# Kernel tuning notes

Measured on AMD Instinct MI355X. Metric: run time of the kernel, lower is better.

The kernel has to match this reference:

```python
import jax, jax.numpy as jnp
import numpy as np

BN_EPS = 1e-5
NEG_SLOPE = 0.2


def _bn(h, gamma, beta, axes):
    # training-mode batch norm over given axes; channels on last axis
    mu = jnp.mean(h, axis=axes, keepdims=True)
    var = jnp.var(h, axis=axes, keepdims=True)
    return (h - mu) * jax.lax.rsqrt(var + BN_EPS) * gamma + beta


def _leaky(h):
    return jnp.where(h >= 0, h, NEG_SLOPE * h)


def setup_inputs() -> dict:
    key = jax.random.key(0)
    k0, k1, k2, k3 = jax.random.split(key, 4)
    B, N, C, K, M = 8, 1024, 512, 20, 64  # M = dim // downrate
    x = jax.random.normal(k0, (B, N, C), dtype=jnp.float32)
    idx = jax.random.randint(k1, (B, N, K), 0, N, dtype=jnp.int32)
    W1 = jax.random.normal(k2, (M, 2 * C), dtype=jnp.float32) * (1.0 / np.sqrt(2 * C))
    gamma1 = jnp.ones((M,), jnp.float32)
    beta1 = jnp.zeros((M,), jnp.float32)
    W2 = jax.random.normal(k3, (C, M), dtype=jnp.float32) * (1.0 / np.sqrt(M))
    gamma2 = jnp.ones((C,), jnp.float32)
    beta2 = jnp.zeros((C,), jnp.float32)
    return dict(x=x, idx=idx, W1=W1, gamma1=gamma1, beta1=beta1,
                W2=W2, gamma2=gamma2, beta2=beta2)


def reference(x, idx, W1, gamma1, beta1, W2, gamma2, beta2):
    # x: (B, N, C) point features; idx: (B, N, K) neighbor indices into N
    neigh = jax.vmap(lambda xb, ib: xb[ib])(x, idx)          # (B, N, K, C) gather
    center = x[:, :, None, :]                                 # (B, N, 1, C)
    # get_graph_feature: concat(feature - x, x) -> channels = 2C
    edge = jnp.concatenate(
        [neigh - center, jnp.broadcast_to(center, neigh.shape)], axis=-1)  # (B,N,K,2C)
    # conv1: 1x1 conv == per-edge linear, then BN2d (stats over B,N,K) + LeakyReLU
    h = jnp.einsum('bnkc,mc->bnkm', edge, W1)                 # (B, N, K, M)
    h = _leaky(_bn(h, gamma1, beta1, (0, 1, 2)))
    # max-aggregate over neighbors
    h = jnp.max(h, axis=2)                                    # (B, N, M)
    # conv2: 1x1 conv1d, BN1d (stats over B,N) + LeakyReLU
    h2 = jnp.einsum('bnm,dm->bnd', h, W2)                     # (B, N, C)
    h2 = _leaky(_bn(h2, gamma2, beta2, (0, 1)))
    return h2  # (B, N, dim), matches final permute(0, 2, 1)
```

## Files before the change

kernel.cpp:

```cpp
#include <hip/hip_runtime.h>
#include <math.h>

#define B_ 8
#define N_ 1024
#define C_ 512
#define K_ 20
#define M_ 64
#define R_ (B_*N_)

typedef short bf16x8 __attribute__((ext_vector_type(8)));
typedef float f32x4  __attribute__((ext_vector_type(4)));

#define WS_Y     0
#define WS_HMM   (WS_Y + R_*64)
#define WS_P1A   (WS_HMM + R_*64)
#define WS_P2A   (WS_P1A + 128)
#define WS_HB    (WS_P2A + 1024)

__device__ __forceinline__ uint f2b(float f) {
    union { float f; uint u; } v; v.f = f;
    return (v.u + 0x7fffu + ((v.u >> 16) & 1u)) >> 16;
}
__device__ __forceinline__ uint2 f4_to_b4(float4 v) {
    uint2 r;
    r.x = f2b(v.x) | (f2b(v.y) << 16);
    r.y = f2b(v.z) | (f2b(v.w) << 16);
    return r;
}
__device__ __forceinline__ float bits2f(uint u) {
    union { uint u; float f; } v; v.u = u; return v.f;
}
__device__ __forceinline__ float lrelu(float v) { return v >= 0.f ? v : 0.2f * v; }

__global__ __launch_bounds__(256) void k_yz(const float* __restrict__ x,
                                            const float* __restrict__ W1,
                                            ushort* __restrict__ Y,
                                            float* __restrict__ P1a,
                                            float* __restrict__ P2a) {
    __shared__ __align__(16) ushort sWb[65536];
    const int t = threadIdx.x, lane = t & 63, w = t >> 6;
    const int wr = w >> 1, wc = w & 1;
    const int r0 = blockIdx.x * 32;

#pragma unroll 8
    for (int i = 0; i < 32; ++i) {
        const int f = i * 256 + t;
        const int j = f >> 6, kq = f & 63;
        const float* src = (j < 64) ? &W1[(size_t)j * 1024 + kq * 8]
                                    : &W1[(size_t)(j - 64) * 1024 + 512 + kq * 8];
        const float4 a = *(const float4*)src;
        const float4 b = *(const float4*)(src + 4);
        const uint2 la = f4_to_b4(a), lb = f4_to_b4(b);
        uint4 v; v.x = la.x; v.y = la.y; v.z = lb.x; v.w = lb.y;
        const int off = j * 1024 + ((kq * 16) ^ ((j & 7) << 4));
        *(uint4*)((char*)sWb + off) = v;
    }
    if (blockIdx.x == 0 && t < 128) P1a[t] = 0.f;
    if (blockIdx.x >= 1 && blockIdx.x <= 4) P2a[(blockIdx.x - 1) * 256 + t] = 0.f;

    const int arow = r0 + wr * 16 + (lane & 15);
    const size_t xbase = (size_t)arow * 512 + ((lane >> 4) * 8);
    float4 xr[8][4];
#pragma unroll
    for (int ks = 0; ks < 8; ++ks) {
        const size_t b = xbase + ks * 64;
        xr[ks][0] = *(const float4*)&x[b];
        xr[ks][1] = *(const float4*)&x[b + 4];
        xr[ks][2] = *(const float4*)&x[b + 32];
        xr[ks][3] = *(const float4*)&x[b + 36];
    }

    f32x4 acc[4];
#pragma unroll
    for (int jj = 0; jj < 4; ++jj) acc[jj] = (f32x4){0.f, 0.f, 0.f, 0.f};

    __syncthreads();

    const int jbase = wc * 64 + (lane & 15);
    const int kb_base = (lane >> 4) * 16;

#pragma unroll
    for (int ks = 0; ks < 8; ++ks) {
        const uint2 c00 = f4_to_b4(xr[ks][0]), c01 = f4_to_b4(xr[ks][1]);
        const uint2 c10 = f4_to_b4(xr[ks][2]), c11 = f4_to_b4(xr[ks][3]);
        union { uint4 u; bf16x8 b; } A0, A1;
        A0.u.x = c00.x; A0.u.y = c00.y; A0.u.z = c01.x; A0.u.w = c01.y;
        A1.u.x = c10.x; A1.u.y = c10.y; A1.u.z = c11.x; A1.u.w = c11.y;
        const int k0 = ks * 128 + kb_base;
#pragma unroll
        for (int jj = 0; jj < 4; ++jj) {
            const int jrow = jbase + jj * 16;
            const int rowoff = jrow * 1024;
            const int sw = (jrow & 7) << 4;
            const bf16x8 B0 = *(const bf16x8*)((char*)sWb + rowoff + (k0 ^ sw));
            const bf16x8 B1 = *(const bf16x8*)((char*)sWb + rowoff + ((k0 + 64) ^ sw));
            acc[jj] = __builtin_amdgcn_mfma_f32_16x16x32_bf16(A0.b, B0, acc[jj], 0, 0, 0);
            acc[jj] = __builtin_amdgcn_mfma_f32_16x16x32_bf16(A1.b, B1, acc[jj], 0, 0, 0);
        }
    }

    const int crow = r0 + wr * 16 + (lane >> 4) * 4;
    const int ccol = wc * 64 + (lane & 15);
#pragma unroll
    for (int jj = 0; jj < 4; ++jj)
#pragma unroll
        for (int i = 0; i < 4; ++i)
            Y[(size_t)(crow + i) * 128 + ccol + jj * 16] = (ushort)f2b(acc[jj][i]);
}

__global__ __launch_bounds__(256) void k_gather(const ushort* __restrict__ Y,
                                                const int* __restrict__ idx,
                                                uint* __restrict__ HMM,
                                                float* __restrict__ P1a) {
    __shared__ float sSum[8][64];
    __shared__ float sQ[8][64];
    const int t = threadIdx.x, lane = t & 63, w = t >> 6;
    const int sub = lane >> 5, c = lane & 31;
    const int grp = w * 2 + sub;
    const uint* Yu = (const uint*)Y;
    float sum0 = 0.f, sum1 = 0.f, sq0 = 0.f, sq1 = 0.f;

#pragma unroll
    for (int pi = 0; pi < 4; ++pi) {
        const int p = blockIdx.x * 32 + w * 8 + pi * 2 + sub;
        const int bb = p >> 10;
        const uint ysu = Yu[(size_t)p * 64 + c];
        const uint zsu = Yu[(size_t)p * 64 + 32 + c];
        const float base0 = bits2f(zsu << 16) - bits2f(ysu << 16);
        const float base1 = bits2f(zsu & 0xffff0000u) - bits2f(ysu & 0xffff0000u);
        float mx0 = -INFINITY, mx1 = -INFINITY, mn0 = INFINITY, mn1 = INFINITY;
        int4 j4[5];
#pragma unroll
        for (int q = 0; q < 5; ++q) j4[q] = *(const int4*)&idx[p * 20 + q * 4];
#pragma unroll
        for (int k = 0; k < 20; ++k) {
            const int j = ((const int*)j4)[k];
            const uint yg = Yu[(size_t)(bb * 1024 + j) * 64 + c];
            const float h0 = bits2f(yg << 16) + base0;
            const float h1 = bits2f(yg & 0xffff0000u) + base1;
            sum0 += h0; sum1 += h1;
            sq0 += h0 * h0; sq1 += h1 * h1;
            mx0 = fmaxf(mx0, h0); mx1 = fmaxf(mx1, h1);
            mn0 = fminf(mn0, h0); mn1 = fminf(mn1, h1);
        }
        uint2 st;
        st.x = f2b(mx0) | (f2b(mn0) << 16);
        st.y = f2b(mx1) | (f2b(mn1) << 16);
        *(uint2*)&HMM[(size_t)p * 64 + 2 * c] = st;
    }

    *(float2*)&sSum[grp][2 * c] = make_float2(sum0, sum1);
    *(float2*)&sQ[grp][2 * c]   = make_float2(sq0, sq1);
    __syncthreads();
    if (t < 64) {
        float s = 0.f, q = 0.f;
#pragma unroll
        for (int g = 0; g < 8; ++g) { s += sSum[g][t]; q += sQ[g][t]; }
        atomicAdd(&P1a[t], s);
        atomicAdd(&P1a[64 + t], q);
    }
}

__global__ __launch_bounds__(256) void k_qsum(const uint* __restrict__ HMM,
                                              const float* __restrict__ P1a,
                                              const float* __restrict__ g1,
                                              const float* __restrict__ b1,
                                              const float* __restrict__ W2,
                                              ushort* __restrict__ Hb,
                                              float* __restrict__ P2a) {
    __shared__ float sSc1[64], sSh1[64];
    const int t = threadIdx.x, lane = t & 63, w = t >> 6;
    if (t < 64) {
        const float inv = 1.f / (float)(R_ * K_);
        const float mu  = P1a[t] * inv;
        const float var = P1a[64 + t] * inv - mu * mu;
        const float rs  = rsqrtf(var + 1e-5f);
        const float sc  = g1[t] * rs;
        sSc1[t] = sc;
        sSh1[t] = b1[t] - mu * sc;
    }
    __syncthreads();

    const int rtile = blockIdx.x, half = blockIdx.y;
    const int r0 = rtile * 64;
    const int dsub = half * 256 + w * 64;
    const int qd = lane >> 4, s = lane & 15;
    const int mc0 = qd * 8;

    bf16x8 bfr[4][2];
#pragma unroll
    for (int f = 0; f < 4; ++f) {
        const int d = dsub + f * 16 + s;
#pragma unroll
        for (int g = 0; g < 2; ++g) {
            const float4 wa = *(const float4*)&W2[(size_t)d * 64 + mc0 + g * 32];
            const float4 wb = *(const float4*)&W2[(size_t)d * 64 + mc0 + g * 32 + 4];
            const uint2 lo = f4_to_b4(wa), hi = f4_to_b4(wb);
            union { uint4 u; bf16x8 b; } cv;
            cv.u.x = lo.x; cv.u.y = lo.y; cv.u.z = hi.x; cv.u.w = hi.y;
            bfr[f][g] = cv.b;
        }
    }

    f32x4 acc[4][4];
#pragma unroll
    for (int rt = 0; rt < 4; ++rt)
#pragma unroll
        for (int f = 0; f < 4; ++f) acc[rt][f] = (f32x4){0.f,0.f,0.f,0.f};

#pragma unroll
    for (int rt = 0; rt < 4; ++rt) {
        const int row = r0 + rt * 16 + s;
#pragma unroll
        for (int g = 0; g < 2; ++g) {
            const int mc = mc0 + g * 32;
            const uint4 u0 = *(const uint4*)&HMM[(size_t)row * 64 + mc];
            const uint4 u1 = *(const uint4*)&HMM[(size_t)row * 64 + mc + 4];
            float v[8];
#pragma unroll
            for (int i = 0; i < 4; ++i) {
                const uint ua = ((const uint*)&u0)[i];
                const uint ub = ((const uint*)&u1)[i];
                const float c0 = sSc1[mc + i],     h0 = sSh1[mc + i];
                const float c4 = sSc1[mc + 4 + i], h4 = sSh1[mc + 4 + i];
                const float a0 = c0 >= 0.f ? bits2f(ua << 16) : bits2f(ua & 0xffff0000u);
                const float a4 = c4 >= 0.f ? bits2f(ub << 16) : bits2f(ub & 0xffff0000u);
                v[i]     = lrelu(a0 * c0 + h0);
                v[i + 4] = lrelu(a4 * c4 + h4);
            }
            uint4 pk;
            pk.x = f2b(v[0]) | (f2b(v[1]) << 16);
            pk.y = f2b(v[2]) | (f2b(v[3]) << 16);
            pk.z = f2b(v[4]) | (f2b(v[5]) << 16);
            pk.w = f2b(v[6]) | (f2b(v[7]) << 16);
            if (half == 0) *(uint4*)&Hb[(size_t)row * 64 + mc] = pk;
            union { uint4 u; bf16x8 b; } cv; cv.u = pk;
#pragma unroll
            for (int f = 0; f < 4; ++f)
                acc[rt][f] = __builtin_amdgcn_mfma_f32_16x16x32_bf16(cv.b, bfr[f][g], acc[rt][f], 0, 0, 0);
        }
    }

#pragma unroll
    for (int f = 0; f < 4; ++f) {
        float ss = 0.f, qq = 0.f;
#pragma unroll
        for (int rt = 0; rt < 4; ++rt)
#pragma unroll
            for (int i = 0; i < 4; ++i) {
                const float vv = acc[rt][f][i];
                ss += vv; qq += vv * vv;
            }
        ss += __shfl_xor(ss, 16); ss += __shfl_xor(ss, 32);
        qq += __shfl_xor(qq, 16); qq += __shfl_xor(qq, 32);
        if (lane < 16) {
            const int d = dsub + f * 16 + s;
            atomicAdd(&P2a[d], ss);
            atomicAdd(&P2a[512 + d], qq);
        }
    }
}

__global__ __launch_bounds__(256) void k_out(const ushort* __restrict__ Hb,
                                             const float* __restrict__ W2,
                                             const float* __restrict__ P2a,
                                             const float* __restrict__ g2,
                                             const float* __restrict__ b2,
                                             float* __restrict__ out) {
    __shared__ float sSc2[256], sSh2[256];
    const int t = threadIdx.x, lane = t & 63, w = t >> 6;
    const int rtile = blockIdx.x, half = blockIdx.y;
    {
        const int d = half * 256 + t;
        const float inv = 1.f / (float)R_;
        const float mu  = P2a[d] * inv;
        const float var = P2a[512 + d] * inv - mu * mu;
        const float rs  = rsqrtf(var + 1e-5f);
        const float sc  = g2[d] * rs;
        sSc2[t] = sc;
        sSh2[t] = b2[d] - mu * sc;
    }
    __syncthreads();

    const int r0 = rtile * 64;
    const int dsub = half * 256 + w * 64;
    const int qd = lane >> 4, s = lane & 15;
    const int mc0 = qd * 8;

    bf16x8 bfr[4][2];
#pragma unroll
    for (int f = 0; f < 4; ++f) {
        const int d = dsub + f * 16 + s;
#pragma unroll
        for (int g = 0; g < 2; ++g) {
            const float4 wa = *(const float4*)&W2[(size_t)d * 64 + mc0 + g * 32];
            const float4 wb = *(const float4*)&W2[(size_t)d * 64 + mc0 + g * 32 + 4];
            const uint2 lo = f4_to_b4(wa), hi = f4_to_b4(wb);
            union { uint4 u; bf16x8 b; } cv;
            cv.u.x = lo.x; cv.u.y = lo.y; cv.u.z = hi.x; cv.u.w = hi.y;
            bfr[f][g] = cv.b;
        }
    }

    f32x4 acc[4][4];
#pragma unroll
    for (int rt = 0; rt < 4; ++rt)
#pragma unroll
        for (int f = 0; f < 4; ++f) acc[rt][f] = (f32x4){0.f,0.f,0.f,0.f};

#pragma unroll
    for (int rt = 0; rt < 4; ++rt) {
        const int row = r0 + rt * 16 + s;
#pragma unroll
        for (int g = 0; g < 2; ++g) {
            const bf16x8 af = *(const bf16x8*)&Hb[(size_t)row * 64 + mc0 + g * 32];
#pragma unroll
            for (int f = 0; f < 4; ++f)
                acc[rt][f] = __builtin_amdgcn_mfma_f32_16x16x32_bf16(af, bfr[f][g], acc[rt][f], 0, 0, 0);
        }
    }

#pragma unroll
    for (int rt = 0; rt < 4; ++rt)
#pragma unroll
        for (int f = 0; f < 4; ++f) {
            const int dl = w * 64 + f * 16 + s;
            const float c2 = sSc2[dl], h2 = sSh2[dl];
            const int d = dsub + f * 16 + s;
#pragma unroll
            for (int i = 0; i < 4; ++i) {
                const float vv = lrelu(acc[rt][f][i] * c2 + h2);
                out[(size_t)(r0 + rt * 16 + qd * 4 + i) * 512 + d] = vv;
            }
        }
}

extern "C" void kernel_launch(void* const* d_in, const int* in_sizes, int n_in,
                              void* d_out, int out_size, void* d_ws, size_t ws_size,
                              hipStream_t stream) {
    const float* x   = (const float*)d_in[0];
    const int*   idx = (const int*)d_in[1];
    const float* W1  = (const float*)d_in[2];
    const float* g1  = (const float*)d_in[3];
    const float* b1  = (const float*)d_in[4];
    const float* W2  = (const float*)d_in[5];
    const float* g2  = (const float*)d_in[6];
    const float* b2  = (const float*)d_in[7];
    float* out = (float*)d_out;
    float* ws  = (float*)d_ws;

    ushort* Y    = (ushort*)(ws + WS_Y);
    uint*   HMM  = (uint*)(ws + WS_HMM);
    float*  P1a  = ws + WS_P1A;
    float*  P2a  = ws + WS_P2A;
    ushort* Hb   = (ushort*)(ws + WS_HB);

    k_yz    <<<dim3(R_ / 32), dim3(256), 0, stream>>>(x, W1, Y, P1a, P2a);
    k_gather<<<dim3(R_ / 32), dim3(256), 0, stream>>>(Y, idx, HMM, P1a);
    k_qsum  <<<dim3(128, 2),  dim3(256), 0, stream>>>(HMM, P1a, g1, b1, W2, Hb, P2a);
    k_out   <<<dim3(128, 2),  dim3(256), 0, stream>>>(Hb, W2, P2a, g2, b2, out);
}
```

Baseline: 52.32 us.

## Stream W1 in double-buffered K-chunks in k_yz with 512-thread blocks

The k_yz GEMM no longer stages the whole 128x512 bf16 W1 tile (128 KB LDS) up front. It now streams 64-wide K slices into a 32 KB double-buffered LDS ring, prefetching the next slice of W1 and x into registers while MFMAs run on the current one. Blocks grow to 512 threads (8 waves, each owning 32 output columns), which cuts LDS use and register pressure so more blocks can be resident. The cost is a __syncthreads per K step and fewer MFMAs per wave between barriers.

```diff
diff --git a/kernel.cpp b/kernel.cpp
--- a/kernel.cpp
+++ b/kernel.cpp
@@ -32,77 +32,116 @@
 }
 __device__ __forceinline__ float lrelu(float v) { return v >= 0.f ? v : 0.2f * v; }
 
-__global__ __launch_bounds__(256) void k_yz(const float* __restrict__ x,
+__global__ __launch_bounds__(512) void k_yz(const float* __restrict__ x,
                                             const float* __restrict__ W1,
                                             ushort* __restrict__ Y,
                                             float* __restrict__ P1a,
                                             float* __restrict__ P2a) {
-    __shared__ __align__(16) ushort sWb[65536];
+    __shared__ __align__(16) char sW[2 * 16384];
     const int t = threadIdx.x, lane = t & 63, w = t >> 6;
-    const int wr = w >> 1, wc = w & 1;
+    const int wr = w >> 2, wc = w & 3;
     const int r0 = blockIdx.x * 32;
 
-#pragma unroll 8
-    for (int i = 0; i < 32; ++i) {
-        const int f = i * 256 + t;
-        const int j = f >> 6, kq = f & 63;
-        const float* src = (j < 64) ? &W1[(size_t)j * 1024 + kq * 8]
-                                    : &W1[(size_t)(j - 64) * 1024 + 512 + kq * 8];
-        const float4 a = *(const float4*)src;
-        const float4 b = *(const float4*)(src + 4);
-        const uint2 la = f4_to_b4(a), lb = f4_to_b4(b);
-        uint4 v; v.x = la.x; v.y = la.y; v.z = lb.x; v.w = lb.y;
-        const int off = j * 1024 + ((kq * 16) ^ ((j & 7) << 4));
-        *(uint4*)((char*)sWb + off) = v;
-    }
     if (blockIdx.x == 0 && t < 128) P1a[t] = 0.f;
-    if (blockIdx.x >= 1 && blockIdx.x <= 4) P2a[(blockIdx.x - 1) * 256 + t] = 0.f;
+    if (blockIdx.x >= 1 && blockIdx.x <= 2) P2a[(blockIdx.x - 1) * 512 + t] = 0.f;
+
+    int srow[2], sslot[2];
+    size_t swsrc[2];
+    int sdst[2];
+#pragma unroll
+    for (int q = 0; q < 2; ++q) {
+        const int f = q * 512 + t;
+        const int row = f >> 3, slot = f & 7;
+        srow[q] = row; sslot[q] = slot;
+        swsrc[q] = (row < 64 ? (size_t)row * 1024 : (size_t)(row - 64) * 1024 + 512)
+                 + slot * 8;
+        sdst[q] = row * 128 + ((slot * 16) ^ ((row & 7) << 4));
+    }
 
     const int arow = r0 + wr * 16 + (lane & 15);
-    const size_t xbase = (size_t)arow * 512 + ((lane >> 4) * 8);
-    float4 xr[8][4];
-#pragma unroll
+    const size_t xrow = (size_t)arow * 512;
+    const int kb = (lane >> 4) * 8;
+
+    int boff[2][2];
+#pragma unroll
+    for (int g = 0; g < 2; ++g)
+#pragma unroll
+        for (int jj = 0; jj < 2; ++jj) {
+            const int jrow = wc * 32 + jj * 16 + (lane & 15);
+            boff[g][jj] = jrow * 128 + ((g * 64 + (lane >> 4) * 16) ^ ((jrow & 7) << 4));
+        }
+
+    float4 sA[2][2], sN[2][2];
+#pragma unroll
+    for (int q = 0; q < 2; ++q) {
+        sA[q][0] = *(const float4*)&W1[swsrc[q]];
+        sA[q][1] = *(const float4*)&W1[swsrc[q] + 4];
+    }
+    float4 xa[4], xn[4];
+    xa[0] = *(const float4*)&x[xrow + kb];
+    xa[1] = *(const float4*)&x[xrow + kb + 4];
+    xa[2] = *(const float4*)&x[xrow + 32 + kb];
+    xa[3] = *(const float4*)&x[xrow + 32 + kb + 4];
+
+#pragma unroll
+    for (int q = 0; q < 2; ++q) {
+        const uint2 lo = f4_to_b4(sA[q][0]), hi = f4_to_b4(sA[q][1]);
+        uint4 v; v.x = lo.x; v.y = lo.y; v.z = hi.x; v.w = hi.y;
+        *(uint4*)(sW + sdst[q]) = v;
+    }
+    __syncthreads();
+
+    f32x4 acc[2];
+    acc[0] = (f32x4){0.f, 0.f, 0.f, 0.f};
+    acc[1] = (f32x4){0.f, 0.f, 0.f, 0.f};
+
     for (int ks = 0; ks < 8; ++ks) {
-        const size_t b = xbase + ks * 64;
-        xr[ks][0] = *(const float4*)&x[b];
-        xr[ks][1] = *(const float4*)&x[b + 4];
-        xr[ks][2] = *(const float4*)&x[b + 32];
-        xr[ks][3] = *(const float4*)&x[b + 36];
-    }
-
-    f32x4 acc[4];
-#pragma unroll
-    for (int jj = 0; jj < 4; ++jj) acc[jj] = (f32x4){0.f, 0.f, 0.f, 0.f};
-
-    __syncthreads();
-
-    const int jbase = wc * 64 + (lane & 15);
-    const int kb_base = (lane >> 4) * 16;
-
-#pragma unroll
-    for (int ks = 0; ks < 8; ++ks) {
-        const uint2 c00 = f4_to_b4(xr[ks][0]), c01 = f4_to_b4(xr[ks][1]);
-        const uint2 c10 = f4_to_b4(xr[ks][2]), c11 = f4_to_b4(xr[ks][3]);
-        union { uint4 u; bf16x8 b; } A0, A1;
-        A0.u.x = c00.x; A0.u.y = c00.y; A0.u.z = c01.x; A0.u.w = c01.y;
-        A1.u.x = c10.x; A1.u.y = c10.y; A1.u.z = c11.x; A1.u.w = c11.y;
-        const int k0 = ks * 128 + kb_base;
-#pragma unroll
-        for (int jj = 0; jj < 4; ++jj) {
-            const int jrow = jbase + jj * 16;
-            const int rowoff = jrow * 1024;
-            const int sw = (jrow & 7) << 4;
-            const bf16x8 B0 = *(const bf16x8*)((char*)sWb + rowoff + (k0 ^ sw));
-            const bf16x8 B1 = *(const bf16x8*)((char*)sWb + rowoff + ((k0 + 64) ^ sw));
-            acc[jj] = __builtin_amdgcn_mfma_f32_16x16x32_bf16(A0.b, B0, acc[jj], 0, 0, 0);
-            acc[jj] = __builtin_amdgcn_mfma_f32_16x16x32_bf16(A1.b, B1, acc[jj], 0, 0, 0);
-        }
+        const int cur = ks & 1;
+        const char* buf = sW + cur * 16384;
+
+        if (ks < 7) {
+            const int k0 = (ks + 1) * 64;
+#pragma unroll
+            for (int q = 0; q < 2; ++q) {
+                sN[q][0] = *(const float4*)&W1[swsrc[q] + k0];
+                sN[q][1] = *(const float4*)&W1[swsrc[q] + k0 + 4];
+            }
+            xn[0] = *(const float4*)&x[xrow + k0 + kb];
+            xn[1] = *(const float4*)&x[xrow + k0 + kb + 4];
+            xn[2] = *(const float4*)&x[xrow + k0 + 32 + kb];
+            xn[3] = *(const float4*)&x[xrow + k0 + 32 + kb + 4];
+        }
+
+#pragma unroll
+        for (int g = 0; g < 2; ++g) {
+            const uint2 c0 = f4_to_b4(xa[g * 2]), c1 = f4_to_b4(xa[g * 2 + 1]);
+            union { uint4 u; bf16x8 b; } A;
+            A.u.x = c0.x; A.u.y = c0.y; A.u.z = c1.x; A.u.w = c1.y;
+#pragma unroll
+            for (int jj = 0; jj < 2; ++jj) {
+                const bf16x8 Bf = *(const bf16x8*)(buf + boff[g][jj]);
+                acc[jj] = __builtin_amdgcn_mfma_f32_16x16x32_bf16(A.b, Bf, acc[jj], 0, 0, 0);
+            }
+        }
+
+        if (ks < 7) {
+            char* nbuf = sW + (cur ^ 1) * 16384;
+#pragma unroll
+            for (int q = 0; q < 2; ++q) {
+                const uint2 lo = f4_to_b4(sN[q][0]), hi = f4_to_b4(sN[q][1]);
+                uint4 v; v.x = lo.x; v.y = lo.y; v.z = hi.x; v.w = hi.y;
+                *(uint4*)(nbuf + sdst[q]) = v;
+            }
+#pragma unroll
+            for (int i = 0; i < 4; ++i) xa[i] = xn[i];
+        }
+        __syncthreads();
     }
 
     const int crow = r0 + wr * 16 + (lane >> 4) * 4;
-    const int ccol = wc * 64 + (lane & 15);
-#pragma unroll
-    for (int jj = 0; jj < 4; ++jj)
+    const int ccol = wc * 32 + (lane & 15);
+#pragma unroll
+    for (int jj = 0; jj < 2; ++jj)
 #pragma unroll
         for (int i = 0; i < 4; ++i)
             Y[(size_t)(crow + i) * 128 + ccol + jj * 16] = (ushort)f2b(acc[jj][i]);
@@ -355,7 +394,7 @@
     float*  P2a  = ws + WS_P2A;
     ushort* Hb   = (ushort*)(ws + WS_HB);
 
-    k_yz    <<<dim3(R_ / 32), dim3(256), 0, stream>>>(x, W1, Y, P1a, P2a);
+    k_yz    <<<dim3(R_ / 32), dim3(512), 0, stream>>>(x, W1, Y, P1a, P2a);
     k_gather<<<dim3(R_ / 32), dim3(256), 0, stream>>>(Y, idx, HMM, P1a);
     k_qsum  <<<dim3(128, 2),  dim3(256), 0, stream>>>(HMM, P1a, g1, b1, W2, Hb, P2a);
     k_out   <<<dim3(128, 2),  dim3(256), 0, stream>>>(Hb, W2, P2a, g2, b2, out);
```

Result: faster. 45.79 us (-12.5%).
